# Kernel optimization log

Measured on AMD Instinct MI355X. Metric: run time of the kernel, lower is better.

Reference implementation:

```python
import jax, jax.numpy as jnp
import numpy as np

H = 512  # hidden_size

def _gru_layer(x_tbf, Wih, Whh, bih, bhh):
    # x_tbf: (T, B, F). PyTorch GRU cell:
    # r = sig(Wir x + bir + Whr h + bhr); z = sig(Wiz x + biz + Whz h + bhz)
    B = x_tbf.shape[1]
    gx = jnp.einsum('tbf,gf->tbg', x_tbf, Wih) + bih  # (T, B, 3H), precomputed input gates
    def step(h, gx_t):
        gh = h @ Whh.T + bhh  # (B, 3H)
        r = jax.nn.sigmoid(gx_t[:, :H] + gh[:, :H])
        z = jax.nn.sigmoid(gx_t[:, H:2*H] + gh[:, H:2*H])
        n = jnp.tanh(gx_t[:, 2*H:] + r * gh[:, 2*H:])
        h_new = (1.0 - z) * n + z * h
        return h_new, h_new
    h0 = jnp.zeros((B, H), dtype=x_tbf.dtype)
    hT, ys = jax.lax.scan(step, h0, gx)
    return ys, hT  # (T, B, H), (B, H)


def setup_inputs() -> dict:
    key = jax.random.key(0)
    ks = jax.random.split(key, 12)
    B, T, I, O = 32, 1024, 128, 128
    k = 1.0 / np.sqrt(H)
    u = lambda kk, shape: jax.random.uniform(kk, shape, jnp.float32, -k, k)
    return {
        'x': jax.random.normal(ks[0], (B, T, I), jnp.float32),
        'Wih0': u(ks[1], (3 * H, I)),
        'Whh0': u(ks[2], (3 * H, H)),
        'bih0': u(ks[3], (3 * H,)),
        'bhh0': u(ks[4], (3 * H,)),
        'Wih1': u(ks[5], (3 * H, H)),
        'Whh1': u(ks[6], (3 * H, H)),
        'bih1': u(ks[7], (3 * H,)),
        'bhh1': u(ks[8], (3 * H,)),
        'Wout': u(ks[9], (O, H)),
        'bout': u(ks[10], (O,)),
    }


def reference(x, Wih0, Whh0, bih0, bhh0, Wih1, Whh1, bih1, bhh1, Wout, bout):
    x_tbf = jnp.transpose(x, (1, 0, 2))  # (T, B, I)
    y0, h0T = _gru_layer(x_tbf, Wih0, Whh0, bih0, bhh0)
    y1, h1T = _gru_layer(y0, Wih1, Whh1, bih1, bhh1)
    # Linear output applied at every timestep
    out = jnp.einsum('tbh,oh->bto', y1, Wout) + bout  # (B, T, O)
    hidden = jnp.stack([h0T, h1T], axis=0)  # (n_layers, B, H)
    return out, hidden
```

## Files before the change

kernel.cpp:

```cpp
#include <hip/hip_runtime.h>


typedef __attribute__((ext_vector_type(8))) short short8;
typedef __attribute__((ext_vector_type(4))) float floatx4;

#define MFMA_BF16(a, b, c) __builtin_amdgcn_mfma_f32_16x16x32_bf16(a, b, c, 0, 0, 0)

#define NWG 130
#define FSTR 16
#define EX_REC 132096
#define EX_OUT 66560
#define HBUF_REC (EX_REC + 24576)
#define LDS_BYTES 157696
#define HID_OFF 4194304
#define SLOT 32768

__device__ __align__(16) unsigned g_flags[4096];
__device__ __align__(16) unsigned short g_y0[33587200];
__device__ __align__(16) unsigned short g_y1[33587200];
__device__ __align__(16) unsigned short g_xf[8388608];

static __device__ __forceinline__ float bf2f(unsigned short u) {
  unsigned v = ((unsigned)u) << 16;
  return __builtin_bit_cast(float, v);
}
static __device__ __forceinline__ unsigned short f2bf(float f) {
  unsigned u = __builtin_bit_cast(unsigned, f);
  u = (u + 0x7fffu + ((u >> 16) & 1u)) >> 16;
  return (unsigned short)u;
}
static __device__ __forceinline__ float sigf(float x) {
  return 1.f / (1.f + __expf(-x));
}
static __device__ __forceinline__ void st8(unsigned short* p, unsigned long long v) {
  __hip_atomic_store((unsigned long long*)p, v, __ATOMIC_RELAXED,
                     __HIP_MEMORY_SCOPE_AGENT);
}
static __device__ __forceinline__ unsigned long long pack4(const unsigned short* u) {
  return (unsigned long long)u[0] | ((unsigned long long)u[1] << 16) |
         ((unsigned long long)u[2] << 32) | ((unsigned long long)u[3] << 48);
}
static __device__ __forceinline__ void ldfrag(const unsigned short* slot, int kb,
                                              int t, int lane, short8& hi,
                                              short8& lo) {
  const unsigned short* base = slot + (kb * 2 + t) * 1024 + lane * 8;
  hi = *(const short8*)base;
  lo = *(const short8*)(base + 512);
}

extern "C" __global__ void gru_init() {
  int i = blockIdx.x * blockDim.x + threadIdx.x;
  if (i < 4096) {
    g_flags[i] = 0u;
  } else if (i < 20480) {
    ((unsigned*)g_y0)[i - 4096] = 0u;
  } else if (i < 36864) {
    ((unsigned*)g_y1)[i - 20480] = 0u;
  }
}

extern "C" __global__ void x_arrange(const float* __restrict__ x) {
  int gid = blockIdx.x * 256 + threadIdx.x;
  int t = gid >> 9;
  int rem = gid & 511;
  int kb = rem >> 7;
  int tile = (rem >> 6) & 1;
  int lane = rem & 63;
  int b = tile * 16 + (lane & 15);
  int k = kb * 32 + (lane >> 4) * 8;
  const float* src = x + b * 131072 + t * 128 + k;
  short8 hi, lo;
#pragma unroll
  for (int e = 0; e < 8; ++e) {
    float v = src[e];
    unsigned short h = f2bf(v);
    hi[e] = (short)h;
    lo[e] = (short)f2bf(v - bf2f(h));
  }
  unsigned short* dst = g_xf + ((t * 4 + kb) * 2 + tile) * 1024;
  *(short8*)(dst + lane * 8) = hi;
  *(short8*)(dst + 512 + lane * 8) = lo;
}

template <int LAYER>
__device__ __forceinline__ void layer_step(
    int i, int tid, int q, int lane, int jb,
    const unsigned short* whi, const unsigned short* wlo, float* ex, float* hbuf,
    float* __restrict__ dout,
    float bsr, float bsz, float bin, float bhn, float& hp) {
  constexpr int IHK = LAYER ? 512 : 128;
  constexpr int IHS = IHK / 32;
  constexpr int KSW = LAYER ? 8 : 5;
  constexpr int WSTR = IHK + 512 + 8;
  const int lm = lane & 15, lq = lane >> 4;

  const unsigned short* ihs = LAYER ? (g_y0 + (size_t)i * SLOT) : nullptr;
  const unsigned short* hhs =
      LAYER ? (g_y1 + (size_t)(i - 1) * SLOT) : (g_y0 + (size_t)i * SLOT);

  const floatx4 z4 = {0.f, 0.f, 0.f, 0.f};
  floatx4 t0h[2] = {z4, z4}, t0l[2] = {z4, z4};
  floatx4 tih_h[2] = {z4, z4}, tih_l[2] = {z4, z4};
  floatx4 thh_h[2] = {z4, z4}, thh_l[2] = {z4, z4};

#pragma unroll
  for (int s = 0; s < KSW; ++s) {
    int ks = q * KSW + s;
    int colk = ks * 32 + lq * 8;
    short8 ah[2], al[2];
    if (ks < IHS) {
      if (LAYER == 0) {
        const unsigned short* xb = g_xf + (i * 4 + ks) * 2048;
        ah[0] = *(const short8*)(xb + lane * 8);
        al[0] = *(const short8*)(xb + 512 + lane * 8);
        ah[1] = *(const short8*)(xb + 1024 + lane * 8);
        al[1] = *(const short8*)(xb + 1536 + lane * 8);
      } else {
        ldfrag(ihs, ks, 0, lane, ah[0], al[0]);
        ldfrag(ihs, ks, 1, lane, ah[1], al[1]);
      }
    } else {
      ldfrag(hhs, ks - IHS, 0, lane, ah[0], al[0]);
      ldfrag(hhs, ks - IHS, 1, lane, ah[1], al[1]);
    }
    short8 b0h = *(const short8*)(whi + lm * WSTR + colk);
    short8 b0l = *(const short8*)(wlo + lm * WSTR + colk);
    short8 b1h = *(const short8*)(whi + (16 + lm) * WSTR + colk);
    short8 b1l = *(const short8*)(wlo + (16 + lm) * WSTR + colk);
#pragma unroll
    for (int t = 0; t < 2; ++t) {
      t0h[t] = MFMA_BF16(ah[t], b0h, t0h[t]);
      t0l[t] = MFMA_BF16(ah[t], b0l, t0l[t]);
      t0l[t] = MFMA_BF16(al[t], b0h, t0l[t]);
      if (ks < IHS) {
        tih_h[t] = MFMA_BF16(ah[t], b1h, tih_h[t]);
        tih_l[t] = MFMA_BF16(ah[t], b1l, tih_l[t]);
        tih_l[t] = MFMA_BF16(al[t], b1h, tih_l[t]);
      } else {
        thh_h[t] = MFMA_BF16(ah[t], b1h, thh_h[t]);
        thh_l[t] = MFMA_BF16(ah[t], b1l, thh_l[t]);
        thh_l[t] = MFMA_BF16(al[t], b1h, thh_l[t]);
      }
    }
  }
#pragma unroll
  for (int t = 0; t < 2; ++t) {
    *(floatx4*)(ex + ((0 * 4 + q) * 2 + t) * 256 + lane * 4) = t0h[t] + t0l[t];
    *(floatx4*)(ex + ((1 * 4 + q) * 2 + t) * 256 + lane * 4) = tih_h[t] + tih_l[t];
    *(floatx4*)(ex + ((2 * 4 + q) * 2 + t) * 256 + lane * 4) = thh_h[t] + thh_l[t];
  }
  __syncthreads();

  int m = tid >> 3, j = tid & 7;
  int quad = (m >> 2) & 3, reg = m & 3, mh = m >> 4;
  int offr = (quad * 16 + j) * 4 + reg;
  int offz = (quad * 16 + 8 + j) * 4 + reg;
  float sr = 0, sz = 0, sih = 0, shh = 0;
#pragma unroll
  for (int qq = 0; qq < 4; ++qq) {
    const float* s0 = ex + ((0 * 4 + qq) * 2 + mh) * 256;
    const float* s1 = ex + ((1 * 4 + qq) * 2 + mh) * 256;
    const float* s2 = ex + ((2 * 4 + qq) * 2 + mh) * 256;
    sr += s0[offr];
    sz += s0[offz];
    sih += s1[offr];
    shh += s2[offr];
  }
  float r = sigf(sr + bsr);
  float z = sigf(sz + bsz);
  float n = tanhf(sih + bin + r * (shh + bhn));
  float h = (1.f - z) * n + z * hp;
  hp = h;
  hbuf[m * 8 + j] = h;
  if (i == (LAYER ? 1024 : 1023))
    dout[HID_OFF + LAYER * 16384 + m * 512 + jb + j] = h;
  __syncthreads();

  if (tid < 32) {
    int mm = tid;
    int t = mm >> 4;
    int lanep = (mm & 15) + 16 * ((jb >> 3) & 3);
    int kb = jb >> 5;
    unsigned short h4[8], l4[8];
#pragma unroll
    for (int e = 0; e < 8; ++e) {
      float v = hbuf[mm * 8 + e];
      unsigned short hh = f2bf(v);
      h4[e] = hh;
      l4[e] = f2bf(v - bf2f(hh));
    }
    unsigned short* slot =
        LAYER ? (g_y1 + (size_t)i * SLOT) : (g_y0 + (size_t)(i + 1) * SLOT);
    unsigned short* p = slot + (kb * 2 + t) * 1024 + lanep * 8;
    st8(p, pack4(h4));
    st8(p + 4, pack4(h4 + 4));
    st8(p + 512, pack4(l4));
    st8(p + 516, pack4(l4 + 4));
  }
}

__device__ __forceinline__ void out_step(
    int i, int tid, int lane, int q, int ob,
    const unsigned short* wl, float* ex,
    float* __restrict__ dout, const float* bo) {
  const int lm = lane & 15, lq = lane >> 4;
  const unsigned short* slot = g_y1 + (size_t)(i - 1) * SLOT;
  const floatx4 z4 = {0.f, 0.f, 0.f, 0.f};
  floatx4 acc[4][2];
#pragma unroll
  for (int nt = 0; nt < 4; ++nt) { acc[nt][0] = z4; acc[nt][1] = z4; }
#pragma unroll
  for (int s = 0; s < 4; ++s) {
    int ks = q * 4 + s;
    int colk = ks * 32 + lq * 8;
    short8 a0 = *(const short8*)(slot + (ks * 2 + 0) * 1024 + lane * 8);
    short8 a1 = *(const short8*)(slot + (ks * 2 + 1) * 1024 + lane * 8);
#pragma unroll
    for (int nt = 0; nt < 4; ++nt) {
      short8 b = *(const short8*)(wl + (nt * 16 + lm) * 520 + colk);
      acc[nt][0] = MFMA_BF16(a0, b, acc[nt][0]);
      acc[nt][1] = MFMA_BF16(a1, b, acc[nt][1]);
    }
  }
#pragma unroll
  for (int nt = 0; nt < 4; ++nt) {
    *(floatx4*)(ex + ((q * 4 + nt) * 2 + 0) * 256 + lane * 4) = acc[nt][0];
    *(floatx4*)(ex + ((q * 4 + nt) * 2 + 1) * 256 + lane * 4) = acc[nt][1];
  }
  __syncthreads();
  int m = tid >> 3, oc = (tid & 7) * 8;
  int t_out = i - 2;
  float sv[8];
#pragma unroll
  for (int k = 0; k < 8; ++k) {
    int o = oc + k;
    int nt = o >> 4, jj = o & 15;
    int off = (((m >> 2) & 3) * 16 + jj) * 4 + (m & 3);
    int mh = m >> 4;
    float s = bo[k];
#pragma unroll
    for (int qq = 0; qq < 4; ++qq) s += ex[((qq * 4 + nt) * 2 + mh) * 256 + off];
    sv[k] = s;
  }
  float* dst = dout + m * 131072 + t_out * 128 + ob + oc;
  *(floatx4*)dst = floatx4{sv[0], sv[1], sv[2], sv[3]};
  *(floatx4*)(dst + 4) = floatx4{sv[4], sv[5], sv[6], sv[7]};
}

extern "C" __global__ void __launch_bounds__(256, 1) gru_main(
    const float* __restrict__ Wih0, const float* __restrict__ Whh0,
    const float* __restrict__ bih0, const float* __restrict__ bhh0,
    const float* __restrict__ Wih1, const float* __restrict__ Whh1,
    const float* __restrict__ bih1, const float* __restrict__ bhh1,
    const float* __restrict__ Wout, const float* __restrict__ boutp,
    float* __restrict__ dout) {
  extern __shared__ char smem[];
  __shared__ int sbail;

  int* flags = (int*)g_flags;

  const int w = blockIdx.x;
  const int tid = threadIdx.x;
  const int lane = tid & 63;
  const int q = tid >> 6;
  const int role = (w < 128) ? ((w < 64) ? 0 : 1) : 2;

  if (tid == 0) sbail = 0;

  unsigned short* whi = (unsigned short*)smem;
  float* ex = (float*)(smem + (role == 2 ? EX_OUT : EX_REC));
  float* hbuf = (float*)(smem + HBUF_REC);
  {
    int exn = (role == 2) ? 8192 : 6144;
    for (int idx = tid; idx < exn; idx += 256) ex[idx] = 0.f;
  }

  float bsr = 0, bsz = 0, bin = 0, bhn = 0;
  float bo[8] = {0, 0, 0, 0, 0, 0, 0, 0};
  int jb = 0, ob = 0;
  const unsigned short* wlo = nullptr;

  if (role < 2) {
    jb = (role == 0 ? w : w - 64) * 8;
    const int IHK = role ? 512 : 128;
    const int KTOT = IHK + 512;
    const int WSTR = KTOT + 8;
    unsigned short* wlo_w = whi + 32 * WSTR;
    wlo = wlo_w;
    const float* Wih = role ? Wih1 : Wih0;
    const float* Whh = role ? Whh1 : Whh0;
    const float* bih = role ? bih1 : bih0;
    const float* bhh = role ? bhh1 : bhh0;
    int cpr = KTOT / 8;
    for (int idx = tid; idx < 32 * cpr; idx += 256) {
      int r = idx / cpr, c = idx - r * cpr;
      int k0 = c * 8;
      short8 hi8 = {0, 0, 0, 0, 0, 0, 0, 0}, lo8 = {0, 0, 0, 0, 0, 0, 0, 0};
      if (r < 24) {
        int gate = r >> 3, jl = r & 7;
        int grow = gate * 512 + jb + jl;
        const float* src = (k0 < IHK) ? (Wih + grow * IHK + k0)
                                      : (Whh + grow * 512 + (k0 - IHK));
#pragma unroll
        for (int e = 0; e < 8; ++e) {
          float v = src[e];
          unsigned short h16 = f2bf(v);
          hi8[e] = (short)h16;
          lo8[e] = (short)f2bf(v - bf2f(h16));
        }
      }
      *(short8*)(whi + r * WSTR + k0) = hi8;
      *(short8*)(wlo_w + r * WSTR + k0) = lo8;
    }
    for (int idx = tid; idx < 32 * 8; idx += 256) {
      int r = idx >> 3, kk = KTOT + (idx & 7);
      whi[r * WSTR + kk] = 0;
      wlo_w[r * WSTR + kk] = 0;
    }
    int g0 = jb + (tid & 7);
    bsr = bih[g0] + bhh[g0];
    bsz = bih[512 + g0] + bhh[512 + g0];
    bin = bih[1024 + g0];
    bhn = bhh[1024 + g0];
  } else {
    ob = (w - 128) * 64;
    for (int idx = tid; idx < 64 * 64; idx += 256) {
      int r = idx >> 6, c = idx & 63;
      const float* src = Wout + (ob + r) * 512 + c * 8;
      short8 hi8;
#pragma unroll
      for (int e = 0; e < 8; ++e) hi8[e] = (short)f2bf(src[e]);
      *(short8*)(whi + r * 520 + c * 8) = hi8;
    }
    for (int idx = tid; idx < 64 * 8; idx += 256)
      whi[(idx >> 3) * 520 + 512 + (idx & 7)] = 0;
#pragma unroll
    for (int k = 0; k < 8; ++k) bo[k] = boutp[ob + (tid & 7) * 8 + k];
  }
  __builtin_amdgcn_fence(__ATOMIC_ACQUIRE, "agent");
  __syncthreads();

  float hp = 0.f;

  for (int i = 0; i < 1026; ++i) {
    if (i > 0 && tid < 64) {
      int guard = 0;
      for (;;) {
        bool ok;
        if (role == 0) {
          ok = __hip_atomic_load(flags + tid * FSTR, __ATOMIC_RELAXED,
                                 __HIP_MEMORY_SCOPE_AGENT) >= i;
        } else if (role == 1) {
          ok = (__hip_atomic_load(flags + tid * FSTR, __ATOMIC_RELAXED,
                                  __HIP_MEMORY_SCOPE_AGENT) >= i) &&
               (__hip_atomic_load(flags + (64 + tid) * FSTR, __ATOMIC_RELAXED,
                                  __HIP_MEMORY_SCOPE_AGENT) >= i);
        } else {
          ok = __hip_atomic_load(flags + (64 + tid) * FSTR, __ATOMIC_RELAXED,
                                 __HIP_MEMORY_SCOPE_AGENT) >= i;
        }
        if (__ballot(ok) == ~0ull) break;
        __builtin_amdgcn_s_sleep(1);
        if (++guard > (1 << 17)) { sbail = 1; break; }
      }
    }
    __syncthreads();
    if (sbail) break;

    bool active = (role == 0) ? (i < 1024)
                : (role == 1) ? (i >= 1 && i < 1025)
                              : (i >= 2);
    if (active) {
      if (role == 0) {
        layer_step<0>(i, tid, q, lane, jb, whi, wlo, ex, hbuf, dout,
                      bsr, bsz, bin, bhn, hp);
      } else if (role == 1) {
        layer_step<1>(i, tid, q, lane, jb, whi, wlo, ex, hbuf, dout,
                      bsr, bsz, bin, bhn, hp);
      } else {
        out_step(i, tid, lane, q, ob, whi, ex, dout, bo);
      }
    }
    __syncthreads();
    if (tid == 0)
      __hip_atomic_store(&flags[w * FSTR], i + 1, __ATOMIC_RELAXED,
                         __HIP_MEMORY_SCOPE_AGENT);
  }
}

extern "C" void kernel_launch(void* const* d_in, const int* in_sizes, int n_in,
                              void* d_out, int out_size, void* d_ws, size_t ws_size,
                              hipStream_t stream) {
  const float* x = (const float*)d_in[0];
  const float* Wih0 = (const float*)d_in[1];
  const float* Whh0 = (const float*)d_in[2];
  const float* bih0 = (const float*)d_in[3];
  const float* bhh0 = (const float*)d_in[4];
  const float* Wih1 = (const float*)d_in[5];
  const float* Whh1 = (const float*)d_in[6];
  const float* bih1 = (const float*)d_in[7];
  const float* bhh1 = (const float*)d_in[8];
  const float* Wout = (const float*)d_in[9];
  const float* bout = (const float*)d_in[10];

  hipLaunchKernelGGL(gru_init, dim3(144), dim3(256), 0, stream);
  hipLaunchKernelGGL(x_arrange, dim3(524288 / 256), dim3(256), 0, stream, x);

  hipFuncSetAttribute((const void*)gru_main,
                      hipFuncAttributeMaxDynamicSharedMemorySize, LDS_BYTES);
  hipLaunchKernelGGL(gru_main, dim3(NWG), dim3(256), LDS_BYTES, stream,
                     Wih0, Whh0, bih0, bhh0, Wih1, Whh1, bih1, bhh1, Wout,
                     bout, (float*)d_out);
}
```

Baseline: 6.310 ms.

## Merge both GRU layers into one workgroup set, keep low weight halves in registers

Each recurrent workgroup now computes both layer 0 and layer 1 for its eight hidden units, which cuts the grid from 130 to 66 workgroups and leaves only 64 flags to poll per step. The low bf16 halves of the split weights move from LDS into per-thread registers so both layers' high halves fit in LDS. The goal is a smaller cross-workgroup barrier and less LDS traffic. In exchange, each workgroup does about twice the serial work per step and register pressure rises sharply, which may cause spills.

Result: slower. 9.424 ms (+49.4%).

```diff
diff --git a/kernel.cpp b/kernel.cpp
--- a/kernel.cpp
+++ b/kernel.cpp
@@ -6,12 +6,13 @@
 
 #define MFMA_BF16(a, b, c) __builtin_amdgcn_mfma_f32_16x16x32_bf16(a, b, c, 0, 0, 0)
 
-#define NWG 130
+#define NWG 66
 #define FSTR 16
-#define EX_REC 132096
+#define W1_OFF 41472
+#define EX_REC 107520
 #define EX_OUT 66560
-#define HBUF_REC (EX_REC + 24576)
-#define LDS_BYTES 157696
+#define HBUF_REC 132096
+#define LDS_BYTES 133120
 #define HID_OFF 4194304
 #define SLOT 32768
 
@@ -82,10 +83,42 @@
   *(short8*)(dst + 512 + lane * 8) = lo;
 }
 
+template <int LAYER, int KSW>
+__device__ __forceinline__ void load_blo(int q, int lane, int jb,
+                                         const float* __restrict__ Wih,
+                                         const float* __restrict__ Whh,
+                                         short8 (*blo)[2]) {
+  constexpr int IHK = LAYER ? 512 : 128;
+  const int lm = lane & 15, lq = lane >> 4;
+#pragma unroll
+  for (int s = 0; s < KSW; ++s) {
+    int ks = q * KSW + s;
+    int colk = ks * 32 + lq * 8;
+#pragma unroll
+    for (int tt = 0; tt < 2; ++tt) {
+      int r = tt * 16 + lm;
+      short8 lo8 = {0, 0, 0, 0, 0, 0, 0, 0};
+      if (r < 24) {
+        int gate = r >> 3, jl = r & 7;
+        int grow = gate * 512 + jb + jl;
+        const float* src = (colk < IHK) ? (Wih + grow * IHK + colk)
+                                        : (Whh + grow * 512 + (colk - IHK));
+#pragma unroll
+        for (int e = 0; e < 8; ++e) {
+          float v = src[e];
+          unsigned short h16 = f2bf(v);
+          lo8[e] = (short)f2bf(v - bf2f(h16));
+        }
+      }
+      blo[s][tt] = lo8;
+    }
+  }
+}
+
 template <int LAYER>
 __device__ __forceinline__ void layer_step(
     int i, int tid, int q, int lane, int jb,
-    const unsigned short* whi, const unsigned short* wlo, float* ex, float* hbuf,
+    const unsigned short* whi, const short8 (*blo)[2], float* ex, float* hbuf,
     float* __restrict__ dout,
     float bsr, float bsz, float bin, float bhn, float& hp) {
   constexpr int IHK = LAYER ? 512 : 128;
@@ -124,9 +157,9 @@
       ldfrag(hhs, ks - IHS, 1, lane, ah[1], al[1]);
     }
     short8 b0h = *(const short8*)(whi + lm * WSTR + colk);
-    short8 b0l = *(const short8*)(wlo + lm * WSTR + colk);
     short8 b1h = *(const short8*)(whi + (16 + lm) * WSTR + colk);
-    short8 b1l = *(const short8*)(wlo + (16 + lm) * WSTR + colk);
+    short8 b0l = blo[s][0];
+    short8 b1l = blo[s][1];
 #pragma unroll
     for (int t = 0; t < 2; ++t) {
       t0h[t] = MFMA_BF16(ah[t], b0h, t0h[t]);
@@ -257,108 +290,97 @@
   extern __shared__ char smem[];
   __shared__ int sbail;
 
-  int* flags = (int*)g_flags;
+  unsigned* flags = g_flags;
 
   const int w = blockIdx.x;
   const int tid = threadIdx.x;
   const int lane = tid & 63;
   const int q = tid >> 6;
-  const int role = (w < 128) ? ((w < 64) ? 0 : 1) : 2;
+  const int role = (w < 64) ? 0 : 1;
 
   if (tid == 0) sbail = 0;
 
-  unsigned short* whi = (unsigned short*)smem;
-  float* ex = (float*)(smem + (role == 2 ? EX_OUT : EX_REC));
+  unsigned short* whi0 = (unsigned short*)smem;
+  unsigned short* whi1 = (unsigned short*)(smem + W1_OFF);
+  float* ex = (float*)(smem + (role ? EX_OUT : EX_REC));
   float* hbuf = (float*)(smem + HBUF_REC);
   {
-    int exn = (role == 2) ? 8192 : 6144;
+    int exn = role ? 8192 : 6144;
     for (int idx = tid; idx < exn; idx += 256) ex[idx] = 0.f;
   }
 
-  float bsr = 0, bsz = 0, bin = 0, bhn = 0;
+  float bsr0 = 0, bsz0 = 0, bin0 = 0, bhn0 = 0;
+  float bsr1 = 0, bsz1 = 0, bin1 = 0, bhn1 = 0;
   float bo[8] = {0, 0, 0, 0, 0, 0, 0, 0};
   int jb = 0, ob = 0;
-  const unsigned short* wlo = nullptr;
-
-  if (role < 2) {
-    jb = (role == 0 ? w : w - 64) * 8;
-    const int IHK = role ? 512 : 128;
-    const int KTOT = IHK + 512;
-    const int WSTR = KTOT + 8;
-    unsigned short* wlo_w = whi + 32 * WSTR;
-    wlo = wlo_w;
-    const float* Wih = role ? Wih1 : Wih0;
-    const float* Whh = role ? Whh1 : Whh0;
-    const float* bih = role ? bih1 : bih0;
-    const float* bhh = role ? bhh1 : bhh0;
-    int cpr = KTOT / 8;
-    for (int idx = tid; idx < 32 * cpr; idx += 256) {
-      int r = idx / cpr, c = idx - r * cpr;
-      int k0 = c * 8;
-      short8 hi8 = {0, 0, 0, 0, 0, 0, 0, 0}, lo8 = {0, 0, 0, 0, 0, 0, 0, 0};
-      if (r < 24) {
-        int gate = r >> 3, jl = r & 7;
-        int grow = gate * 512 + jb + jl;
-        const float* src = (k0 < IHK) ? (Wih + grow * IHK + k0)
-                                      : (Whh + grow * 512 + (k0 - IHK));
-#pragma unroll
-        for (int e = 0; e < 8; ++e) {
-          float v = src[e];
-          unsigned short h16 = f2bf(v);
-          hi8[e] = (short)h16;
-          lo8[e] = (short)f2bf(v - bf2f(h16));
+  short8 blo0[5][2];
+  short8 blo1[8][2];
+
+  if (role == 0) {
+    jb = w * 8;
+    for (int L = 0; L < 2; ++L) {
+      const int IHK = L ? 512 : 128;
+      const int KTOT = IHK + 512;
+      const int WSTR = KTOT + 8;
+      unsigned short* dst = L ? whi1 : whi0;
+      const float* Wih = L ? Wih1 : Wih0;
+      const float* Whh = L ? Whh1 : Whh0;
+      int cpr = KTOT / 8;
+      for (int idx = tid; idx < 32 * cpr; idx += 256) {
+        int rr = idx / cpr, c = idx - rr * cpr;
+        int k0 = c * 8;
+        short8 hi8 = {0, 0, 0, 0, 0, 0, 0, 0};
+        if (rr < 24) {
+          int gate = rr >> 3, jl = rr & 7;
+          int grow = gate * 512 + jb + jl;
+          const float* src = (k0 < IHK) ? (Wih + grow * IHK + k0)
+                                        : (Whh + grow * 512 + (k0 - IHK));
+#pragma unroll
+          for (int e = 0; e < 8; ++e) hi8[e] = (short)f2bf(src[e]);
         }
+        *(short8*)(dst + rr * WSTR + k0) = hi8;
       }
-      *(short8*)(whi + r * WSTR + k0) = hi8;
-      *(short8*)(wlo_w + r * WSTR + k0) = lo8;
-    }
-    for (int idx = tid; idx < 32 * 8; idx += 256) {
-      int r = idx >> 3, kk = KTOT + (idx & 7);
-      whi[r * WSTR + kk] = 0;
-      wlo_w[r * WSTR + kk] = 0;
-    }
+      for (int idx = tid; idx < 32 * 8; idx += 256)
+        dst[(idx >> 3) * WSTR + KTOT + (idx & 7)] = 0;
+    }
+    load_blo<0, 5>(q, lane, jb, Wih0, Whh0, blo0);
+    load_blo<1, 8>(q, lane, jb, Wih1, Whh1, blo1);
     int g0 = jb + (tid & 7);
-    bsr = bih[g0] + bhh[g0];
-    bsz = bih[512 + g0] + bhh[512 + g0];
-    bin = bih[1024 + g0];
-    bhn = bhh[1024 + g0];
+    bsr0 = bih0[g0] + bhh0[g0];
+    bsz0 = bih0[512 + g0] + bhh0[512 + g0];
+    bin0 = bih0[1024 + g0];
+    bhn0 = bhh0[1024 + g0];
+    bsr1 = bih1[g0] + bhh1[g0];
+    bsz1 = bih1[512 + g0] + bhh1[512 + g0];
+    bin1 = bih1[1024 + g0];
+    bhn1 = bhh1[1024 + g0];
   } else {
-    ob = (w - 128) * 64;
+    ob = (w - 64) * 64;
+    unsigned short* wout_l = (unsigned short*)smem;
     for (int idx = tid; idx < 64 * 64; idx += 256) {
       int r = idx >> 6, c = idx & 63;
       const float* src = Wout + (ob + r) * 512 + c * 8;
       short8 hi8;
 #pragma unroll
       for (int e = 0; e < 8; ++e) hi8[e] = (short)f2bf(src[e]);
-      *(short8*)(whi + r * 520 + c * 8) = hi8;
+      *(short8*)(wout_l + r * 520 + c * 8) = hi8;
     }
     for (int idx = tid; idx < 64 * 8; idx += 256)
-      whi[(idx >> 3) * 520 + 512 + (idx & 7)] = 0;
+      wout_l[(idx >> 3) * 520 + 512 + (idx & 7)] = 0;
 #pragma unroll
     for (int k = 0; k < 8; ++k) bo[k] = boutp[ob + (tid & 7) * 8 + k];
   }
   __builtin_amdgcn_fence(__ATOMIC_ACQUIRE, "agent");
   __syncthreads();
 
-  float hp = 0.f;
+  float hp0 = 0.f, hp1 = 0.f;
 
   for (int i = 0; i < 1026; ++i) {
     if (i > 0 && tid < 64) {
       int guard = 0;
       for (;;) {
-        bool ok;
-        if (role == 0) {
-          ok = __hip_atomic_load(flags + tid * FSTR, __ATOMIC_RELAXED,
-                                 __HIP_MEMORY_SCOPE_AGENT) >= i;
-        } else if (role == 1) {
-          ok = (__hip_atomic_load(flags + tid * FSTR, __ATOMIC_RELAXED,
-                                  __HIP_MEMORY_SCOPE_AGENT) >= i) &&
-               (__hip_atomic_load(flags + (64 + tid) * FSTR, __ATOMIC_RELAXED,
-                                  __HIP_MEMORY_SCOPE_AGENT) >= i);
-        } else {
-          ok = __hip_atomic_load(flags + (64 + tid) * FSTR, __ATOMIC_RELAXED,
-                                 __HIP_MEMORY_SCOPE_AGENT) >= i;
-        }
+        bool ok = __hip_atomic_load(flags + lane * FSTR, __ATOMIC_RELAXED,
+                                    __HIP_MEMORY_SCOPE_AGENT) >= (unsigned)i;
         if (__ballot(ok) == ~0ull) break;
         __builtin_amdgcn_s_sleep(1);
         if (++guard > (1 << 17)) { sbail = 1; break; }
@@ -367,23 +389,20 @@
     __syncthreads();
     if (sbail) break;
 
-    bool active = (role == 0) ? (i < 1024)
-                : (role == 1) ? (i >= 1 && i < 1025)
-                              : (i >= 2);
-    if (active) {
-      if (role == 0) {
-        layer_step<0>(i, tid, q, lane, jb, whi, wlo, ex, hbuf, dout,
-                      bsr, bsz, bin, bhn, hp);
-      } else if (role == 1) {
-        layer_step<1>(i, tid, q, lane, jb, whi, wlo, ex, hbuf, dout,
-                      bsr, bsz, bin, bhn, hp);
-      } else {
-        out_step(i, tid, lane, q, ob, whi, ex, dout, bo);
-      }
+    if (role == 0) {
+      if (i < 1024)
+        layer_step<0>(i, tid, q, lane, jb, whi0, blo0, ex, hbuf, dout,
+                      bsr0, bsz0, bin0, bhn0, hp0);
+      if (i >= 1 && i < 1025)
+        layer_step<1>(i, tid, q, lane, jb, whi1, blo1, ex, hbuf, dout,
+                      bsr1, bsz1, bin1, bhn1, hp1);
+    } else {
+      if (i >= 2)
+        out_step(i, tid, lane, q, ob, (unsigned short*)smem, ex, dout, bo);
     }
     __syncthreads();
-    if (tid == 0)
-      __hip_atomic_store(&flags[w * FSTR], i + 1, __ATOMIC_RELAXED,
+    if (tid == 0 && role == 0)
+      __hip_atomic_store(&flags[w * FSTR], (unsigned)(i + 1), __ATOMIC_RELAXED,
                          __HIP_MEMORY_SCOPE_AGENT);
   }
 }
```

## Replace per-step global barrier with fine-grained per-k-slice flag polling

Applied to the files above, without the earlier changes.

Removes the wavefront-0 poll plus __syncthreads at the top of every timestep. Each wave now waits only for the four producer workgroups whose hidden-state slice it is about to load, so MFMA work on slices that are already ready can start while other producers are still finishing. Producers publish their flag right after their own stores drain, instead of after a trailing block barrier. In exchange there are more poll loops spread across waves, the flag store relies on s_waitcnt for ordering, and the shared bail-out path is gone.

Result: slower. 6.471 ms (+2.6%).

```diff
diff --git a/kernel.cpp b/kernel.cpp
--- a/kernel.cpp
+++ b/kernel.cpp
@@ -19,6 +19,21 @@
 __device__ __align__(16) unsigned short g_y0[33587200];
 __device__ __align__(16) unsigned short g_y1[33587200];
 __device__ __align__(16) unsigned short g_xf[8388608];
+
+#define POLL(m, fbase, kb, tgt)                                               \
+  if ((((m) >> (4 * (kb))) & 0xFull) != 0xFull) {                             \
+    int guard_ = 0;                                                           \
+    for (;;) {                                                                \
+      unsigned v_ = __hip_atomic_load((fbase) + lane * FSTR,                  \
+                                      __ATOMIC_RELAXED,                       \
+                                      __HIP_MEMORY_SCOPE_AGENT);              \
+      (m) = __ballot(v_ >= (tgt));                                            \
+      if ((((m) >> (4 * (kb))) & 0xFull) == 0xFull) break;                    \
+      __builtin_amdgcn_s_sleep(1);                                            \
+      if (++guard_ > (1 << 17)) break;                                        \
+    }                                                                         \
+    asm volatile("" ::: "memory");                                            \
+  }
 
 static __device__ __forceinline__ float bf2f(unsigned short u) {
   unsigned v = ((unsigned)u) << 16;
@@ -87,12 +102,18 @@
     int i, int tid, int q, int lane, int jb,
     const unsigned short* whi, const unsigned short* wlo, float* ex, float* hbuf,
     float* __restrict__ dout,
-    float bsr, float bsz, float bin, float bhn, float& hp) {
+    float bsr, float bsz, float bin, float bhn, float& hp,
+    unsigned* flags, unsigned* myflag) {
   constexpr int IHK = LAYER ? 512 : 128;
   constexpr int IHS = IHK / 32;
   constexpr int KSW = LAYER ? 8 : 5;
   constexpr int WSTR = IHK + 512 + 8;
   const int lm = lane & 15, lq = lane >> 4;
+  const unsigned tgt = (unsigned)i;
+
+  const unsigned* f0 = flags;
+  const unsigned* f1 = flags + 64 * FSTR;
+  unsigned long long m0 = 0, m1 = 0;
 
   const unsigned short* ihs = LAYER ? (g_y0 + (size_t)i * SLOT) : nullptr;
   const unsigned short* hhs =
@@ -116,10 +137,16 @@
         ah[1] = *(const short8*)(xb + 1024 + lane * 8);
         al[1] = *(const short8*)(xb + 1536 + lane * 8);
       } else {
+        POLL(m0, f0, ks, tgt);
         ldfrag(ihs, ks, 0, lane, ah[0], al[0]);
         ldfrag(ihs, ks, 1, lane, ah[1], al[1]);
       }
     } else {
+      if (LAYER == 0) {
+        POLL(m0, f0, ks - IHS, tgt);
+      } else {
+        POLL(m1, f1, ks - IHS, tgt);
+      }
       ldfrag(hhs, ks - IHS, 0, lane, ah[0], al[0]);
       ldfrag(hhs, ks - IHS, 1, lane, ah[1], al[1]);
     }
@@ -197,13 +224,22 @@
     st8(p + 512, pack4(l4));
     st8(p + 516, pack4(l4 + 4));
   }
+  if ((tid >> 6) == 0) {
+    asm volatile("s_waitcnt vmcnt(0)" ::: "memory");
+    if (tid == 0)
+      __hip_atomic_store(myflag, (unsigned)(i + 1), __ATOMIC_RELAXED,
+                         __HIP_MEMORY_SCOPE_AGENT);
+  }
 }
 
 __device__ __forceinline__ void out_step(
     int i, int tid, int lane, int q, int ob,
     const unsigned short* wl, float* ex,
-    float* __restrict__ dout, const float* bo) {
+    float* __restrict__ dout, const float* bo, unsigned* flags) {
   const int lm = lane & 15, lq = lane >> 4;
+  const unsigned tgt = (unsigned)i;
+  const unsigned* f1 = flags + 64 * FSTR;
+  unsigned long long m1 = 0;
   const unsigned short* slot = g_y1 + (size_t)(i - 1) * SLOT;
   const floatx4 z4 = {0.f, 0.f, 0.f, 0.f};
   floatx4 acc[4][2];
@@ -213,6 +249,7 @@
   for (int s = 0; s < 4; ++s) {
     int ks = q * 4 + s;
     int colk = ks * 32 + lq * 8;
+    POLL(m1, f1, ks, tgt);
     short8 a0 = *(const short8*)(slot + (ks * 2 + 0) * 1024 + lane * 8);
     short8 a1 = *(const short8*)(slot + (ks * 2 + 1) * 1024 + lane * 8);
 #pragma unroll
@@ -255,17 +292,14 @@
     const float* __restrict__ Wout, const float* __restrict__ boutp,
     float* __restrict__ dout) {
   extern __shared__ char smem[];
-  __shared__ int sbail;
-
-  int* flags = (int*)g_flags;
+
+  unsigned* flags = g_flags;
 
   const int w = blockIdx.x;
   const int tid = threadIdx.x;
   const int lane = tid & 63;
   const int q = tid >> 6;
   const int role = (w < 128) ? ((w < 64) ? 0 : 1) : 2;
-
-  if (tid == 0) sbail = 0;
 
   unsigned short* whi = (unsigned short*)smem;
   float* ex = (float*)(smem + (role == 2 ? EX_OUT : EX_REC));
@@ -343,48 +377,24 @@
   float hp = 0.f;
 
   for (int i = 0; i < 1026; ++i) {
-    if (i > 0 && tid < 64) {
-      int guard = 0;
-      for (;;) {
-        bool ok;
-        if (role == 0) {
-          ok = __hip_atomic_load(flags + tid * FSTR, __ATOMIC_RELAXED,
-                                 __HIP_MEMORY_SCOPE_AGENT) >= i;
-        } else if (role == 1) {
-          ok = (__hip_atomic_load(flags + tid * FSTR, __ATOMIC_RELAXED,
-                                  __HIP_MEMORY_SCOPE_AGENT) >= i) &&
-               (__hip_atomic_load(flags + (64 + tid) * FSTR, __ATOMIC_RELAXED,
-                                  __HIP_MEMORY_SCOPE_AGENT) >= i);
-        } else {
-          ok = __hip_atomic_load(flags + (64 + tid) * FSTR, __ATOMIC_RELAXED,
-                                 __HIP_MEMORY_SCOPE_AGENT) >= i;
-        }
-        if (__ballot(ok) == ~0ull) break;
-        __builtin_amdgcn_s_sleep(1);
-        if (++guard > (1 << 17)) { sbail = 1; break; }
-      }
-    }
-    __syncthreads();
-    if (sbail) break;
-
     bool active = (role == 0) ? (i < 1024)
                 : (role == 1) ? (i >= 1 && i < 1025)
                               : (i >= 2);
     if (active) {
       if (role == 0) {
         layer_step<0>(i, tid, q, lane, jb, whi, wlo, ex, hbuf, dout,
-                      bsr, bsz, bin, bhn, hp);
+                      bsr, bsz, bin, bhn, hp, flags, &flags[w * FSTR]);
       } else if (role == 1) {
         layer_step<1>(i, tid, q, lane, jb, whi, wlo, ex, hbuf, dout,
-                      bsr, bsz, bin, bhn, hp);
+                      bsr, bsz, bin, bhn, hp, flags, &flags[w * FSTR]);
       } else {
-        out_step(i, tid, lane, q, ob, whi, ex, dout, bo);
+        out_step(i, tid, lane, q, ob, whi, ex, dout, bo, flags);
       }
+    } else if (role < 2 && tid == 0) {
+      __hip_atomic_store(&flags[w * FSTR], (unsigned)(i + 1), __ATOMIC_RELAXED,
+                         __HIP_MEMORY_SCOPE_AGENT);
     }
     __syncthreads();
-    if (tid == 0)
-      __hip_atomic_store(&flags[w * FSTR], i + 1, __ATOMIC_RELAXED,
-                         __HIP_MEMORY_SCOPE_AGENT);
   }
 }
 
```
